# Kernel optimization log

Measured on AMD Instinct MI355X. Metric: run time of the kernel, lower is better.

Reference implementation:

```python
import jax, jax.numpy as jnp
import numpy as np

B, S, D = 2, 2048, 1024
H, HD = 16, 64

def setup_inputs() -> dict:
    key = jax.random.key(0)
    ks = jax.random.split(key, 5)
    scale = 1.0 / np.sqrt(D)
    x = jax.random.normal(ks[0], (B, S, D), dtype=jnp.float32)
    wq = jax.random.normal(ks[1], (D, H * HD), dtype=jnp.float32) * scale
    wk = jax.random.normal(ks[2], (D, H * HD), dtype=jnp.float32) * scale
    wv = jax.random.normal(ks[3], (D, H * HD), dtype=jnp.float32) * scale
    wo = jax.random.normal(ks[4], (H * HD, D), dtype=jnp.float32) * scale
    zeros = jnp.zeros((H * HD,), dtype=jnp.float32)
    return {"x": x, "wq": wq, "bq": zeros, "wk": wk, "bk": zeros,
            "wv": wv, "bv": zeros, "wo": wo, "bo": jnp.zeros((D,), jnp.float32)}

def reference(x, wq, bq, wk, bk, wv, bv, wo, bo):
    b, s, _ = x.shape
    att_scale = HD ** -0.5
    # QKV projections -> [b, h, s, hd]
    q = (x @ wq + bq).reshape(b, s, H, HD).transpose(0, 2, 1, 3)
    k = (x @ wk + bk).reshape(b, s, H, HD).transpose(0, 2, 1, 3)
    v = (x @ wv + bv).reshape(b, s, H, HD).transpose(0, 2, 1, 3)
    scores = jnp.einsum('bhqd,bhkd->bhqk', q, k) * att_scale
    weights = jax.nn.softmax(scores, axis=-1)
    out = jnp.einsum('bhqk,bhkd->bhqd', weights, v)
    out = out.transpose(0, 2, 1, 3).reshape(b, s, H * HD)
    return out @ wo + bo
```

## Files before the change

kernel.cpp:

```cpp
#include <hip/hip_runtime.h>
#include <hip/hip_bf16.h>

#define B_  2
#define S_  2048
#define D_  1024
#define H_  16
#define HD_ 64
#define M_  (B_*S_)

using bf16x8 = __attribute__((ext_vector_type(8))) short;
using f32x4  = __attribute__((ext_vector_type(4))) float;
using f32x16 = __attribute__((ext_vector_type(16))) float;
using u32x4  = __attribute__((ext_vector_type(4))) unsigned int;
using uint2v = __attribute__((ext_vector_type(2))) unsigned int;

static __device__ __forceinline__ ushort f2bf(float f) {
    __hip_bfloat16 h = __float2bfloat16(f);
    return *reinterpret_cast<ushort*>(&h);
}
static __device__ __forceinline__ float max3f(float a, float b, float c) {
    return fmaxf(fmaxf(a, b), c);
}
static __device__ __forceinline__ float fexp2(float x) {
#if __has_builtin(__builtin_amdgcn_exp2f)
    return __builtin_amdgcn_exp2f(x);
#else
    return exp2f(x);
#endif
}
static __device__ __forceinline__ unsigned int pack_bf16(float p0, float p1) {
    unsigned int a = __float_as_uint(p0), b = __float_as_uint(p1);
    a += 0x7fffu + ((a >> 16) & 1u);
    b += 0x7fffu + ((b >> 16) & 1u);
    return (a >> 16) | (b & 0xffff0000u);
}

#define GLDS16(gp, lp) __builtin_amdgcn_global_load_lds( \
    (const __attribute__((address_space(1))) void*)(gp), \
    (__attribute__((address_space(3))) void*)(lp), 16, 0, 0)

__global__ void convert_f32_bf16(const float* __restrict__ src, ushort* __restrict__ dst, int n) {
    int i = (blockIdx.x * blockDim.x + threadIdx.x) * 4;
    if (i < n) {
        float4 v = *reinterpret_cast<const float4*>(src + i);
        ushort4 o;
        o.x = f2bf(v.x); o.y = f2bf(v.y); o.z = f2bf(v.z); o.w = f2bf(v.w);
        *reinterpret_cast<ushort4*>(dst + i) = o;
    }
}

__global__ void transpose_w4(const float* __restrict__ wq, const float* __restrict__ wk,
                             const float* __restrict__ wv, const float* __restrict__ wo,
                             ushort* __restrict__ wqkvT, ushort* __restrict__ woT) {
    const int z = blockIdx.z;
    const float* src = (z == 0) ? wq : (z == 1) ? wk : (z == 2) ? wv : wo;
    ushort* dst = (z < 3) ? (wqkvT + (size_t)z * 1024 * 1024) : woT;
    const int R = 1024, C = 1024;
    __shared__ float t[32][33];
    int c0 = blockIdx.x * 32, r0 = blockIdx.y * 32;
    int tx = threadIdx.x, ty = threadIdx.y;
    #pragma unroll
    for (int i = 0; i < 4; i++)
        t[ty + i*8][tx] = src[(size_t)(r0 + ty + i*8) * C + c0 + tx];
    __syncthreads();
    #pragma unroll
    for (int i = 0; i < 4; i++)
        dst[(size_t)(c0 + ty + i*8) * R + r0 + tx] = f2bf(t[tx][ty + i*8]);
}

__global__ void transpose_v(const ushort* __restrict__ src, ushort* __restrict__ dst) {
    __shared__ ushort t[64][72];
    int bh = blockIdx.y, s0 = blockIdx.x * 64;
    #pragma unroll
    for (int p = 0; p < 2; p++) {
        int idx = threadIdx.x + p * 256;
        int r = idx >> 3, cu = (idx & 7) * 8;
        uint4 v = *reinterpret_cast<const uint4*>(src + (size_t)bh * 131072 + (size_t)(s0 + r) * 64 + cu);
        ushort tmp[8];
        *reinterpret_cast<uint4*>(tmp) = v;
        #pragma unroll
        for (int j = 0; j < 8; j++) t[cu + j][r] = tmp[j];
    }
    __syncthreads();
    #pragma unroll
    for (int p = 0; p < 2; p++) {
        int idx = threadIdx.x + p * 256;
        int r = idx >> 3, cu = (idx & 7) * 8;
        *reinterpret_cast<uint4*>(dst + (size_t)bh * 131072 + (size_t)r * S_ + s0 + cu) =
            *reinterpret_cast<uint4*>(&t[r][cu]);
    }
}

template<int MODE>
__launch_bounds__(256, 2)
__global__ void gemm_bt(const ushort* __restrict__ A, const ushort* __restrict__ Bt,
                        int Mdim, int Ndim, int Kdim,
                        ushort* __restrict__ qout, ushort* __restrict__ kout, ushort* __restrict__ vout,
                        const float* __restrict__ bq, const float* __restrict__ bk, const float* __restrict__ bv,
                        float* __restrict__ out, const float* __restrict__ bias)
{
    __shared__ __align__(16) ushort As[2][128][64];
    __shared__ __align__(16) ushort Bs[2][128][64];
    const int tid  = threadIdx.x;
    const int lane = tid & 63, wave = tid >> 6;
    const int wm = wave & 1, wn = wave >> 1;
    const int m0 = blockIdx.y * 128, n0 = blockIdx.x * 128;
    const int g = lane >> 4, c = lane & 15;

    f32x4 acc[4][4];
    #pragma unroll
    for (int i = 0; i < 4; i++)
        #pragma unroll
        for (int j = 0; j < 4; j++) acc[i][j] = (f32x4){0.f, 0.f, 0.f, 0.f};

    const int arow  = lane >> 3;
    const int aslot = (lane & 7) ^ arow;
    const ushort* Ag = A  + (size_t)(m0 + arow) * Kdim + aslot * 8;
    const ushort* Bg = Bt + (size_t)(n0 + arow) * Kdim + aslot * 8;

    auto stage = [&](int buf, int kt) {
        #pragma unroll
        for (int p = 0; p < 4; p++) {
            int ch = wave + p * 4;
            GLDS16(Ag + (size_t)(ch*8) * Kdim + kt, &As[buf][ch*8][0]);
            GLDS16(Bg + (size_t)(ch*8) * Kdim + kt, &Bs[buf][ch*8][0]);
        }
    };

    auto compute = [&](int buf) {
        #pragma unroll
        for (int ks = 0; ks < 2; ks++) {
            bf16x8 af[4], bfr[4];
            #pragma unroll
            for (int t = 0; t < 4; t++) {
                int sl = ((ks*4 + g) ^ (c & 7)) * 8;
                af[t]  = *reinterpret_cast<const bf16x8*>(&As[buf][wm*64 + t*16 + c][sl]);
                bfr[t] = *reinterpret_cast<const bf16x8*>(&Bs[buf][wn*64 + t*16 + c][sl]);
            }
            #pragma unroll
            for (int i = 0; i < 4; i++)
                #pragma unroll
                for (int j = 0; j < 4; j++)
                    acc[i][j] = __builtin_amdgcn_mfma_f32_16x16x32_bf16(af[i], bfr[j], acc[i][j], 0, 0, 0);
        }
    };

    const int NT = Kdim >> 6;
    stage(0, 0);
    __syncthreads();
    #pragma unroll 1
    for (int it = 0; it < NT - 1; ++it) {
        stage((it + 1) & 1, (it + 1) * 64);
        compute(it & 1);
        __syncthreads();
    }
    compute((NT - 1) & 1);

    const float qscale = 0.125f * 1.4426950408889634f;
    #pragma unroll
    for (int i = 0; i < 4; i++) {
      #pragma unroll
      for (int j = 0; j < 4; j++) {
        #pragma unroll
        for (int r = 0; r < 4; r++) {
            int row = m0 + wm*64 + i*16 + g*4 + r;
            int col = n0 + wn*64 + j*16 + c;
            float v = acc[i][j][r];
            if (MODE == 0) {
                int which = col >> 10;
                int cc = col & 1023;
                int b = row >> 11, s = row & 2047;
                int h = cc >> 6, hd = cc & 63;
                size_t dst = (((size_t)(b*H_ + h)) * S_ + s) * HD_ + hd;
                if (which == 0)      qout[dst] = f2bf((v + bq[cc]) * qscale);
                else if (which == 1) kout[dst] = f2bf(v + bk[cc]);
                else                 vout[dst] = f2bf(v + bv[cc]);
            } else {
                out[(size_t)row * Ndim + col] = v + bias[col];
            }
        }
      }
    }
}

__launch_bounds__(512, 4)
__global__ void attn_kernel(const ushort* __restrict__ Q, const ushort* __restrict__ K,
                            const ushort* __restrict__ Vt, ushort* __restrict__ O)
{
    __shared__ __align__(16) ushort Ks[2][2][64][64];
    __shared__ __align__(16) ushort Vs[2][2][64][64];
    const int tid = threadIdx.x, lane = tid & 63, w = tid >> 6;
    const int grp = w >> 2, wq4 = w & 3;
    const int q31 = lane & 31, hi = lane >> 5, x7 = lane & 7;

    int lin = blockIdx.x + gridDim.x * blockIdx.y;
    int xcd = lin & 7, idx = lin >> 3;
    int bh = xcd * 4 + (idx & 3);
    int qb = idx >> 2;
    const int q0 = qb * 128;
    const int kt_base = grp * 1024;
    const ushort* Kp = K  + (size_t)bh * S_ * HD_;
    const ushort* Vp = Vt + (size_t)bh * HD_ * S_;

    bf16x8 qf[4];
    #pragma unroll
    for (int c4 = 0; c4 < 4; c4++)
        qf[c4] = *reinterpret_cast<const bf16x8*>(
            Q + (size_t)bh * S_ * HD_ + (size_t)(q0 + wq4*32 + q31) * HD_ + c4*16 + hi*8);

    f32x16 acc0, acc1;
    #pragma unroll
    for (int r = 0; r < 16; r++) { acc0[r] = 0.f; acc1[r] = 0.f; }
    float m_i = -INFINITY, l_i = 0.f;

    const int srow  = lane >> 3;
    const int sslot = (lane & 7) ^ srow;
    const ushort* kg = Kp + (size_t)srow * HD_ + sslot * 8;
    const ushort* vg = Vp + (size_t)srow * S_  + sslot * 8;

    auto stage = [&](int buf, int kt) {
        #pragma unroll
        for (int p = 0; p < 2; p++) {
            int ch = wq4 + p * 4;
            GLDS16(kg + (size_t)(kt + ch*8) * HD_, &Ks[grp][buf][ch*8][0]);
            GLDS16(vg + (size_t)(ch*8) * S_ + kt,  &Vs[grp][buf][ch*8][0]);
        }
    };

    auto softmax_pack = [&](const f32x16& st, bf16x8& pf0, bf16x8& pf1) {
        float g0 = max3f(st[0],  st[1],  st[2]);
        float g1 = max3f(st[3],  st[4],  st[5]);
        float g2 = max3f(st[6],  st[7],  st[8]);
        float g3 = max3f(st[9],  st[10], st[11]);
        float g4 = max3f(st[12], st[13], st[14]);
        float pm = fmaxf(max3f(g0, g1, g2), max3f(g3, g4, st[15]));
#if __has_builtin(__builtin_amdgcn_permlane32_swap)
        {
            uint2v r = __builtin_amdgcn_permlane32_swap(__float_as_uint(pm), __float_as_uint(pm), false, false);
            pm = fmaxf(__uint_as_float(r.x), __uint_as_float(r.y));
        }
#else
        pm = fmaxf(pm, __shfl_xor(pm, 32));
#endif
        if (__any(pm > m_i + 8.f)) {
            float mnew = fmaxf(m_i, pm);
            float al = fexp2(m_i - mnew);
            l_i *= al;
            #pragma unroll
            for (int r = 0; r < 16; r++) { acc0[r] *= al; acc1[r] *= al; }
            m_i = mnew;
        }
        float rs = 0.f;
        unsigned int dd[8];
        #pragma unroll
        for (int r2 = 0; r2 < 8; r2++) {
            float p0 = fexp2(st[r2*2]     - m_i);
            float p1 = fexp2(st[r2*2 + 1] - m_i);
            rs += p0 + p1;
            dd[r2] = pack_bf16(p0, p1);
        }
#if __has_builtin(__builtin_amdgcn_permlane32_swap)
        {
            uint2v r = __builtin_amdgcn_permlane32_swap(__float_as_uint(rs), __float_as_uint(rs), false, false);
            rs = __uint_as_float(r.x) + __uint_as_float(r.y);
        }
#else
        rs += __shfl_xor(rs, 32);
#endif
        l_i += rs;
        u32x4 t0, t1;
#if __has_builtin(__builtin_amdgcn_permlane32_swap)
        {
            uint2v s02 = __builtin_amdgcn_permlane32_swap(dd[0], dd[2], false, false);
            uint2v s13 = __builtin_amdgcn_permlane32_swap(dd[1], dd[3], false, false);
            uint2v s46 = __builtin_amdgcn_permlane32_swap(dd[4], dd[6], false, false);
            uint2v s57 = __builtin_amdgcn_permlane32_swap(dd[5], dd[7], false, false);
            t0 = (u32x4){s02.x, s13.x, s02.y, s13.y};
            t1 = (u32x4){s46.x, s57.x, s46.y, s57.y};
        }
#else
        {
            unsigned int ee[8];
            #pragma unroll
            for (int r2 = 0; r2 < 8; r2++)
                ee[r2] = (unsigned int)__shfl_xor((int)dd[r2], 32);
            t0 = (u32x4){ hi ? ee[2] : dd[0], hi ? ee[3] : dd[1],
                          hi ? dd[2] : ee[0], hi ? dd[3] : ee[1] };
            t1 = (u32x4){ hi ? ee[6] : dd[4], hi ? ee[7] : dd[5],
                          hi ? dd[6] : ee[4], hi ? dd[7] : ee[5] };
        }
#endif
        pf0 = *reinterpret_cast<bf16x8*>(&t0);
        pf1 = *reinterpret_cast<bf16x8*>(&t1);
    };

    auto compute64 = [&](int buf) {
        const ushort (*ks)[64] = Ks[grp][buf];
        const ushort (*vs)[64] = Vs[grp][buf];
        f32x16 st0, st1;
        #pragma unroll
        for (int r = 0; r < 16; r++) { st0[r] = 0.f; st1[r] = 0.f; }
        __builtin_amdgcn_s_setprio(1);
        #pragma unroll
        for (int c4 = 0; c4 < 4; c4++) {
            bf16x8 kf = *reinterpret_cast<const bf16x8*>(&ks[q31][((c4*2 + hi) ^ x7) * 8]);
            st0 = __builtin_amdgcn_mfma_f32_32x32x16_bf16(kf, qf[c4], st0, 0, 0, 0);
        }
        #pragma unroll
        for (int c4 = 0; c4 < 4; c4++) {
            bf16x8 kf = *reinterpret_cast<const bf16x8*>(&ks[32 + q31][((c4*2 + hi) ^ x7) * 8]);
            st1 = __builtin_amdgcn_mfma_f32_32x32x16_bf16(kf, qf[c4], st1, 0, 0, 0);
        }
        __builtin_amdgcn_s_setprio(0);

        bf16x8 pf0, pf1;
        softmax_pack(st0, pf0, pf1);
        {
            bf16x8 vf0 = *reinterpret_cast<const bf16x8*>(&vs[q31]     [((0 + hi) ^ x7) * 8]);
            bf16x8 vf1 = *reinterpret_cast<const bf16x8*>(&vs[q31]     [((2 + hi) ^ x7) * 8]);
            bf16x8 vf2 = *reinterpret_cast<const bf16x8*>(&vs[32 + q31][((0 + hi) ^ x7) * 8]);
            bf16x8 vf3 = *reinterpret_cast<const bf16x8*>(&vs[32 + q31][((2 + hi) ^ x7) * 8]);
            __builtin_amdgcn_s_setprio(1);
            acc0 = __builtin_amdgcn_mfma_f32_32x32x16_bf16(vf0, pf0, acc0, 0, 0, 0);
            acc0 = __builtin_amdgcn_mfma_f32_32x32x16_bf16(vf1, pf1, acc0, 0, 0, 0);
            acc1 = __builtin_amdgcn_mfma_f32_32x32x16_bf16(vf2, pf0, acc1, 0, 0, 0);
            acc1 = __builtin_amdgcn_mfma_f32_32x32x16_bf16(vf3, pf1, acc1, 0, 0, 0);
            __builtin_amdgcn_s_setprio(0);
        }
        softmax_pack(st1, pf0, pf1);
        {
            bf16x8 vf0 = *reinterpret_cast<const bf16x8*>(&vs[q31]     [((4 + hi) ^ x7) * 8]);
            bf16x8 vf1 = *reinterpret_cast<const bf16x8*>(&vs[q31]     [((6 + hi) ^ x7) * 8]);
            bf16x8 vf2 = *reinterpret_cast<const bf16x8*>(&vs[32 + q31][((4 + hi) ^ x7) * 8]);
            bf16x8 vf3 = *reinterpret_cast<const bf16x8*>(&vs[32 + q31][((6 + hi) ^ x7) * 8]);
            __builtin_amdgcn_s_setprio(1);
            acc0 = __builtin_amdgcn_mfma_f32_32x32x16_bf16(vf0, pf0, acc0, 0, 0, 0);
            acc0 = __builtin_amdgcn_mfma_f32_32x32x16_bf16(vf1, pf1, acc0, 0, 0, 0);
            acc1 = __builtin_amdgcn_mfma_f32_32x32x16_bf16(vf2, pf0, acc1, 0, 0, 0);
            acc1 = __builtin_amdgcn_mfma_f32_32x32x16_bf16(vf3, pf1, acc1, 0, 0, 0);
            __builtin_amdgcn_s_setprio(0);
        }
    };

    stage(0, kt_base);
    __syncthreads();
    #pragma unroll 1
    for (int it = 0; it < 15; ++it) {
        stage((it & 1) ^ 1, kt_base + (it + 1) * 64);
        compute64(it & 1);
        __syncthreads();
    }
    compute64(1);

    __syncthreads();
    float* fb = (wq4 < 2) ? reinterpret_cast<float*>(&Ks[0][0][0][0])
                          : reinterpret_cast<float*>(&Vs[0][0][0][0]);
    const int slot = ((wq4 & 1) * 64 + lane) * 35;
    if (grp == 1) {
        #pragma unroll
        for (int r = 0; r < 16; r++) { fb[slot + r] = acc0[r]; fb[slot + 16 + r] = acc1[r]; }
        fb[slot + 32] = m_i;
        fb[slot + 33] = l_i;
    }
    __syncthreads();
    if (grp == 0) {
        float m2 = fb[slot + 32], l2 = fb[slot + 33];
        float mm = fmaxf(m_i, m2);
        float a1 = fexp2(m_i - mm), a2 = fexp2(m2 - mm);
        float inv = 1.f / (l_i * a1 + l2 * a2);
        const int b = bh >> 4, h = bh & 15;
        const int s = q0 + wq4*32 + q31;
        ushort* op = O + (size_t)(b*S_ + s) * 1024 + h*64;
        #pragma unroll
        for (int rg = 0; rg < 4; rg++) {
            int hd0 = rg*8 + hi*4;
            ushort4 o;
            o.x = f2bf((acc0[rg*4+0]*a1 + fb[slot + rg*4+0]*a2) * inv);
            o.y = f2bf((acc0[rg*4+1]*a1 + fb[slot + rg*4+1]*a2) * inv);
            o.z = f2bf((acc0[rg*4+2]*a1 + fb[slot + rg*4+2]*a2) * inv);
            o.w = f2bf((acc0[rg*4+3]*a1 + fb[slot + rg*4+3]*a2) * inv);
            *reinterpret_cast<ushort4*>(op + hd0) = o;
            o.x = f2bf((acc1[rg*4+0]*a1 + fb[slot + 16 + rg*4+0]*a2) * inv);
            o.y = f2bf((acc1[rg*4+1]*a1 + fb[slot + 16 + rg*4+1]*a2) * inv);
            o.z = f2bf((acc1[rg*4+2]*a1 + fb[slot + 16 + rg*4+2]*a2) * inv);
            o.w = f2bf((acc1[rg*4+3]*a1 + fb[slot + 16 + rg*4+3]*a2) * inv);
            *reinterpret_cast<ushort4*>(op + 32 + hd0) = o;
        }
    }
}

extern "C" void kernel_launch(void* const* d_in, const int* in_sizes, int n_in,
                              void* d_out, int out_size, void* d_ws, size_t ws_size,
                              hipStream_t stream)
{
    const float* x  = (const float*)d_in[0];
    const float* wq = (const float*)d_in[1];
    const float* bq = (const float*)d_in[2];
    const float* wk = (const float*)d_in[3];
    const float* bk = (const float*)d_in[4];
    const float* wv = (const float*)d_in[5];
    const float* bv = (const float*)d_in[6];
    const float* wo = (const float*)d_in[7];
    const float* bo = (const float*)d_in[8];
    float* out = (float*)d_out;

    char* ws = (char*)d_ws;
    ushort* xb    = (ushort*)(ws);
    ushort* wqkvT = (ushort*)(ws + (8ull  << 20));
    ushort* woT   = (ushort*)(ws + (14ull << 20));
    ushort* qw    = (ushort*)(ws + (16ull << 20));
    ushort* kw    = (ushort*)(ws + (24ull << 20));
    ushort* vw    = (ushort*)(ws + (32ull << 20));
    ushort* ao    = (ushort*)(ws + (40ull << 20));
    ushort* vtw   = xb;

    convert_f32_bf16<<<4096, 256, 0, stream>>>(x, xb, M_ * D_);
    transpose_w4<<<dim3(32, 32, 4), dim3(32, 8), 0, stream>>>(wq, wk, wv, wo, wqkvT, woT);

    gemm_bt<0><<<dim3(24, 32), 256, 0, stream>>>(xb, wqkvT, M_, 3072, 1024,
                                                 qw, kw, vw, bq, bk, bv, nullptr, nullptr);
    transpose_v<<<dim3(32, 32), 256, 0, stream>>>(vw, vtw);
    attn_kernel<<<dim3(16, 32), 512, 0, stream>>>(qw, kw, vtw, ao);
    gemm_bt<1><<<dim3(8, 32), 256, 0, stream>>>(ao, woT, M_, 1024, 1024,
                                                nullptr, nullptr, nullptr, nullptr, nullptr, nullptr,
                                                out, bo);
}
```

Measured before the change: 232.3 us.

## Swizzle GEMM tiles per XCD, single-buffer LDS, and hoist epilogue bias/index math

The GEMM grid becomes one-dimensional and block indices are remapped so that blocks on the same XCD work on neighbouring tiles, which should improve L2 reuse of A and B panels. The LDS double buffer becomes a single buffer with load, sync, compute, sync per K-step. That halves shared memory, which may raise occupancy, but global-load latency is no longer overlapped with MFMA work inside a block. The epilogue is also restructured so the q/k/v destination, bias and scale are chosen once per wave rather than per element.

```diff
diff --git a/kernel.cpp b/kernel.cpp
--- a/kernel.cpp
+++ b/kernel.cpp
@@ -99,12 +99,17 @@
                         const float* __restrict__ bq, const float* __restrict__ bk, const float* __restrict__ bv,
                         float* __restrict__ out, const float* __restrict__ bias)
 {
-    __shared__ __align__(16) ushort As[2][128][64];
-    __shared__ __align__(16) ushort Bs[2][128][64];
+    __shared__ __align__(16) ushort As[128][64];
+    __shared__ __align__(16) ushort Bs[128][64];
     const int tid  = threadIdx.x;
     const int lane = tid & 63, wave = tid >> 6;
     const int wm = wave & 1, wn = wave >> 1;
-    const int m0 = blockIdx.y * 128, n0 = blockIdx.x * 128;
+    const int lin = blockIdx.x;
+    const int xcd = lin & 7, idx = lin >> 3;
+    int my, nx;
+    if (MODE == 0) { my = (xcd >> 1) * 8 + idx / 12; nx = (xcd & 1) * 12 + idx % 12; }
+    else           { my = xcd * 4 + (idx >> 3);      nx = idx & 7; }
+    const int m0 = my * 128, n0 = nx * 128;
     const int g = lane >> 4, c = lane & 15;
 
     f32x4 acc[4][4];
@@ -118,24 +123,23 @@
     const ushort* Ag = A  + (size_t)(m0 + arow) * Kdim + aslot * 8;
     const ushort* Bg = Bt + (size_t)(n0 + arow) * Kdim + aslot * 8;
 
-    auto stage = [&](int buf, int kt) {
+    #pragma unroll 1
+    for (int kt = 0; kt < Kdim; kt += 64) {
         #pragma unroll
         for (int p = 0; p < 4; p++) {
             int ch = wave + p * 4;
-            GLDS16(Ag + (size_t)(ch*8) * Kdim + kt, &As[buf][ch*8][0]);
-            GLDS16(Bg + (size_t)(ch*8) * Kdim + kt, &Bs[buf][ch*8][0]);
-        }
-    };
-
-    auto compute = [&](int buf) {
+            GLDS16(Ag + (size_t)(ch*8) * Kdim + kt, &As[ch*8][0]);
+            GLDS16(Bg + (size_t)(ch*8) * Kdim + kt, &Bs[ch*8][0]);
+        }
+        __syncthreads();
         #pragma unroll
         for (int ks = 0; ks < 2; ks++) {
             bf16x8 af[4], bfr[4];
             #pragma unroll
             for (int t = 0; t < 4; t++) {
                 int sl = ((ks*4 + g) ^ (c & 7)) * 8;
-                af[t]  = *reinterpret_cast<const bf16x8*>(&As[buf][wm*64 + t*16 + c][sl]);
-                bfr[t] = *reinterpret_cast<const bf16x8*>(&Bs[buf][wn*64 + t*16 + c][sl]);
+                af[t]  = *reinterpret_cast<const bf16x8*>(&As[wm*64 + t*16 + c][sl]);
+                bfr[t] = *reinterpret_cast<const bf16x8*>(&Bs[wn*64 + t*16 + c][sl]);
             }
             #pragma unroll
             for (int i = 0; i < 4; i++)
@@ -143,43 +147,46 @@
                 for (int j = 0; j < 4; j++)
                     acc[i][j] = __builtin_amdgcn_mfma_f32_16x16x32_bf16(af[i], bfr[j], acc[i][j], 0, 0, 0);
         }
-    };
-
-    const int NT = Kdim >> 6;
-    stage(0, 0);
-    __syncthreads();
-    #pragma unroll 1
-    for (int it = 0; it < NT - 1; ++it) {
-        stage((it + 1) & 1, (it + 1) * 64);
-        compute(it & 1);
         __syncthreads();
     }
-    compute((NT - 1) & 1);
 
     const float qscale = 0.125f * 1.4426950408889634f;
-    #pragma unroll
-    for (int i = 0; i < 4; i++) {
-      #pragma unroll
-      for (int j = 0; j < 4; j++) {
-        #pragma unroll
-        for (int r = 0; r < 4; r++) {
-            int row = m0 + wm*64 + i*16 + g*4 + r;
-            int col = n0 + wn*64 + j*16 + c;
-            float v = acc[i][j][r];
-            if (MODE == 0) {
-                int which = col >> 10;
-                int cc = col & 1023;
+    if (MODE == 0) {
+        const int which = n0 >> 10;
+        const int cc0 = (n0 & 1023) + wn*64;
+        const int h = cc0 >> 6;
+        ushort* dst0 = (which == 0) ? qout : (which == 1) ? kout : vout;
+        const float* bp = (which == 0) ? bq : (which == 1) ? bk : bv;
+        const float scl = (which == 0) ? qscale : 1.f;
+        float bj[4];
+        #pragma unroll
+        for (int j = 0; j < 4; j++) bj[j] = bp[cc0 + j*16 + c];
+        #pragma unroll
+        for (int i = 0; i < 4; i++) {
+            #pragma unroll
+            for (int r = 0; r < 4; r++) {
+                int row = m0 + wm*64 + i*16 + g*4 + r;
                 int b = row >> 11, s = row & 2047;
-                int h = cc >> 6, hd = cc & 63;
-                size_t dst = (((size_t)(b*H_ + h)) * S_ + s) * HD_ + hd;
-                if (which == 0)      qout[dst] = f2bf((v + bq[cc]) * qscale);
-                else if (which == 1) kout[dst] = f2bf(v + bk[cc]);
-                else                 vout[dst] = f2bf(v + bv[cc]);
-            } else {
-                out[(size_t)row * Ndim + col] = v + bias[col];
+                ushort* orow = dst0 + (((size_t)(b*H_ + h)) * S_ + s) * HD_;
+                #pragma unroll
+                for (int j = 0; j < 4; j++)
+                    orow[j*16 + c] = f2bf((acc[i][j][r] + bj[j]) * scl);
             }
         }
-      }
+    } else {
+        float bj[4];
+        #pragma unroll
+        for (int j = 0; j < 4; j++) bj[j] = bias[n0 + wn*64 + j*16 + c];
+        #pragma unroll
+        for (int i = 0; i < 4; i++)
+            #pragma unroll
+            for (int r = 0; r < 4; r++) {
+                int row = m0 + wm*64 + i*16 + g*4 + r;
+                float* orow = out + (size_t)row * Ndim + n0 + wn*64;
+                #pragma unroll
+                for (int j = 0; j < 4; j++)
+                    orow[j*16 + c] = acc[i][j][r] + bj[j];
+            }
     }
 }
 
@@ -417,11 +424,11 @@
     convert_f32_bf16<<<4096, 256, 0, stream>>>(x, xb, M_ * D_);
     transpose_w4<<<dim3(32, 32, 4), dim3(32, 8), 0, stream>>>(wq, wk, wv, wo, wqkvT, woT);
 
-    gemm_bt<0><<<dim3(24, 32), 256, 0, stream>>>(xb, wqkvT, M_, 3072, 1024,
-                                                 qw, kw, vw, bq, bk, bv, nullptr, nullptr);
+    gemm_bt<0><<<768, 256, 0, stream>>>(xb, wqkvT, M_, 3072, 1024,
+                                        qw, kw, vw, bq, bk, bv, nullptr, nullptr);
     transpose_v<<<dim3(32, 32), 256, 0, stream>>>(vw, vtw);
     attn_kernel<<<dim3(16, 32), 512, 0, stream>>>(qw, kw, vtw, ao);
-    gemm_bt<1><<<dim3(8, 32), 256, 0, stream>>>(ao, woT, M_, 1024, 1024,
-                                                nullptr, nullptr, nullptr, nullptr, nullptr, nullptr,
-                                                out, bo);
-}
+    gemm_bt<1><<<256, 256, 0, stream>>>(ao, woT, M_, 1024, 1024,
+                                        nullptr, nullptr, nullptr, nullptr, nullptr, nullptr,
+                                        out, bo);
+}
```

After: 204.8 us. -11.8%, faster.
